# Kernel tuning notes

Measured on AMD Instinct MI355X. Metric: run time of the kernel, lower is better.

Reference implementation:

```python
import jax, jax.numpy as jnp
import numpy as np

DIM = 1024
NUM_HEADS = 16
HEAD_DIM = DIM // NUM_HEADS


def setup_inputs() -> dict:
    key = jax.random.key(0)
    ks = jax.random.split(key, 5)
    scale = 1.0 / np.sqrt(DIM)
    return {
        "x": jax.random.normal(ks[0], (2, 2048, DIM), dtype=jnp.float32),
        "qkv_w": jax.random.normal(ks[1], (3 * DIM, DIM), dtype=jnp.float32) * scale,
        "qkv_b": jax.random.normal(ks[2], (3 * DIM,), dtype=jnp.float32) * 0.01,
        "proj_w": jax.random.normal(ks[3], (DIM, DIM), dtype=jnp.float32) * scale,
        "proj_b": jax.random.normal(ks[4], (DIM,), dtype=jnp.float32) * 0.01,
    }


def reference(x, qkv_w, qkv_b, proj_w, proj_b):
    B, N, D = x.shape
    H, Hd = NUM_HEADS, HEAD_DIM
    # fused QKV projection: [B,N,3D]
    qkv = jnp.einsum('bnd,ed->bne', x, qkv_w) + qkv_b
    qkv = qkv.reshape(B, N, 3, H, Hd)
    q = qkv[:, :, 0].transpose(0, 2, 1, 3)  # [B,H,N,Hd]
    k = qkv[:, :, 1].transpose(0, 2, 1, 3)
    v = qkv[:, :, 2].transpose(0, 2, 1, 3)
    scale = 1.0 / jnp.sqrt(jnp.asarray(Hd, dtype=x.dtype))
    scores = jnp.einsum('bhqd,bhkd->bhqk', q, k) * scale  # [B,H,N,N]
    attn = jax.nn.softmax(scores, axis=-1)
    out = jnp.einsum('bhqk,bhkd->bhqd', attn, v)  # [B,H,N,Hd]
    out = out.transpose(0, 2, 1, 3).reshape(B, N, D)
    return jnp.einsum('bnd,ed->bne', out, proj_w) + proj_b
```

## Files before the change

kernel.cpp:

```cpp
#include <hip/hip_runtime.h>
#include <hip/hip_bf16.h>
#include <stdint.h>


typedef __bf16 bf16;
typedef __bf16 bf16x4 __attribute__((ext_vector_type(4)));
typedef __bf16 bf16x8 __attribute__((ext_vector_type(8)));
typedef float  f32x4  __attribute__((ext_vector_type(4)));
typedef float  f32x16 __attribute__((ext_vector_type(16)));
typedef uint32_t u32x4 __attribute__((ext_vector_type(4)));

#define QSCALE 0.18033688011112042f

__device__ __forceinline__ void gload_lds16(const void* g, void* l) {
    __builtin_amdgcn_global_load_lds(
        (const __attribute__((address_space(1))) void*)(uintptr_t)g,
        (__attribute__((address_space(3))) void*)(uint32_t)(uintptr_t)l,
        16, 0, 0);
}

__device__ __forceinline__ uint32_t pkbf(float a, float b) {
    uint16_t lo = __builtin_bit_cast(uint16_t, (bf16)a);
    uint16_t hi = __builtin_bit_cast(uint16_t, (bf16)b);
    return (uint32_t)lo | ((uint32_t)hi << 16);
}

__global__ void cast_f32_bf16(const float* __restrict__ in, bf16* __restrict__ out, int n4) {
    int i = blockIdx.x * blockDim.x + threadIdx.x;
    if (i < n4) {
        float4 v = ((const float4*)in)[i];
        bf16x4 o = { (bf16)v.x, (bf16)v.y, (bf16)v.z, (bf16)v.w };
        ((bf16x4*)out)[i] = o;
    }
}

template<int EPI>
__global__ __launch_bounds__(256) void gemm128(
    const bf16* __restrict__ A,
    const bf16* __restrict__ Bw,
    const float* __restrict__ bias,
    float* __restrict__ outF,
    bf16* __restrict__ qb, bf16* __restrict__ kf, bf16* __restrict__ vf,
    int K)
{
    __shared__ bf16 As[128 * 32];
    __shared__ bf16 Bs[128 * 32];
    __shared__ bf16 ct[EPI == 0 ? 128 * 144 : 1];
    const int tid  = threadIdx.x;
    const int lane = tid & 63, w = tid >> 6;
    const int g = lane >> 4, lr = lane & 15;
    const int wr = w >> 1, wc = w & 1;
    const int mbase = blockIdx.y * 128, nbase = blockIdx.x * 128;

    f32x4 acc[4][4] = {};

    const bf16* Ag = A  + (size_t)mbase * K;
    const bf16* Bg = Bw + (size_t)nbase * K;

    for (int kt = 0; kt < K; kt += 32) {
        {
            int c0 = tid;
            gload_lds16(Ag + (size_t)(c0 >> 2) * K + (c0 & 3) * 8, As + c0 * 8);
            gload_lds16(Bg + (size_t)(c0 >> 2) * K + (c0 & 3) * 8, Bs + c0 * 8);
            int c1 = 256 + tid;
            gload_lds16(Ag + (size_t)(c1 >> 2) * K + (c1 & 3) * 8, As + c1 * 8);
            gload_lds16(Bg + (size_t)(c1 >> 2) * K + (c1 & 3) * 8, Bs + c1 * 8);
        }
        __syncthreads();
        bf16x8 af[4], bfr[4];
        #pragma unroll
        for (int mi = 0; mi < 4; ++mi)
            af[mi] = *(const bf16x8*)(As + (wr * 64 + mi * 16 + lr) * 32 + g * 8);
        #pragma unroll
        for (int ni = 0; ni < 4; ++ni)
            bfr[ni] = *(const bf16x8*)(Bs + (wc * 64 + ni * 16 + lr) * 32 + g * 8);
        #pragma unroll
        for (int mi = 0; mi < 4; ++mi)
            #pragma unroll
            for (int ni = 0; ni < 4; ++ni)
                acc[mi][ni] = __builtin_amdgcn_mfma_f32_16x16x32_bf16(
                    af[mi], bfr[ni], acc[mi][ni], 0, 0, 0);
        __syncthreads();
        Ag += 32; Bg += 32;
    }

    if (EPI == 1) {
        #pragma unroll
        for (int ni = 0; ni < 4; ++ni) {
            int e = nbase + wc * 64 + ni * 16 + lr;
            float bv = bias[e];
            #pragma unroll
            for (int mi = 0; mi < 4; ++mi) {
                #pragma unroll
                for (int r = 0; r < 4; ++r) {
                    int token = mbase + wr * 64 + mi * 16 + g * 4 + r;
                    outF[(size_t)token * 1024 + e] = acc[mi][ni][r] + bv;
                }
            }
        }
    } else {
        const int sec = nbase >> 10;
        #pragma unroll
        for (int ni = 0; ni < 4; ++ni) {
            int ec = wc * 64 + ni * 16 + lr;
            float bv = bias[nbase + ec];
            #pragma unroll
            for (int mi = 0; mi < 4; ++mi) {
                #pragma unroll
                for (int r = 0; r < 4; ++r) {
                    int tl = wr * 64 + mi * 16 + g * 4 + r;
                    float v = acc[mi][ni][r] + bv;
                    if (sec == 0) v *= QSCALE;
                    int row = (sec == 2) ? ec : tl;
                    int col = (sec == 2) ? tl : ec;
                    ct[row * 144 + col] = (bf16)v;
                }
            }
        }
        __syncthreads();
        const int b  = mbase >> 11;
        const int h0 = (nbase & 1023) >> 6;
        const int mb = mbase & 2047;
        #pragma unroll
        for (int si = 0; si < 8; ++si) {
            int c   = si * 256 + tid;
            int hh  = c >> 10;
            int w10 = c & 1023;
            int bh  = b * 16 + h0 + hh;
            int lrow, lcol;
            size_t gaddr;
            bf16* dst;
            if (sec == 0) {
                int nl = w10 >> 3, d0 = (w10 & 7) * 8;
                lrow = nl; lcol = hh * 64 + d0;
                gaddr = ((size_t)bh * 2048 + mb + nl) * 64 + d0;
                dst = qb;
            } else if (sec == 1) {
                int o = w10 * 8;
                int frag = o >> 9, l = (o >> 3) & 63;
                int nl = (frag >> 2) * 32 + (l & 31);
                int d0 = (frag & 3) * 16 + (l >> 5) * 8;
                lrow = nl; lcol = hh * 64 + d0;
                gaddr = ((size_t)(bh * 64 + (mb >> 5))) * 2048 + o;
                dst = kf;
            } else {
                int o = w10 * 8;
                int n6 = o >> 12, r2 = o & 4095;
                int d5 = r2 >> 11, r3 = r2 & 2047;
                int nc = r3 >> 9,  l  = (r3 >> 3) & 63;
                int d  = d5 * 32 + (l & 31);
                int n0 = n6 * 64 + nc * 16 + (l >> 5) * 8;
                lrow = hh * 64 + d; lcol = n0;
                gaddr = ((size_t)(bh * 32 + (mb >> 6))) * 4096 + o;
                dst = vf;
            }
            *(bf16x8*)(dst + gaddr) = *(const bf16x8*)(&ct[lrow * 144 + lcol]);
        }
    }
}

__global__ __launch_bounds__(256, 2) void attn32(
    const bf16* __restrict__ Q,
    const bf16* __restrict__ Kf,
    const bf16* __restrict__ Vf,
    bf16* __restrict__ Ao,
    int Nseq)
{
    __shared__ bf16 Ks[2][4096];
    __shared__ bf16 Vs[2][4096];
    __shared__ bf16 ot[4][32][66];
    const int tid  = threadIdx.x;
    const int lane = tid & 63, w = tid >> 6;
    const int hi = lane >> 5, ql = lane & 31;
    const int bid = blockIdx.x;
    const int xcd = bid & 7, ii = bid >> 3;
    const int bh = xcd * 4 + (ii >> 4), qc = ii & 15;
    const int h = bh & 15, b = bh >> 4;
    const int q0 = qc * 128 + w * 32;

    const bf16* Qh  = Q  + (size_t)bh * Nseq * 64;
    const bf16* Kfh = Kf + (size_t)bh * Nseq * 64;
    const bf16* Vfh = Vf + (size_t)bh * Nseq * 64;

    bf16x8 qf[4];
    #pragma unroll
    for (int c = 0; c < 4; ++c)
        qf[c] = *(const bf16x8*)(Qh + (size_t)(q0 + ql) * 64 + c * 16 + hi * 8);

    f32x16 o0 = {}, o1 = {};
    f32x16 lv = {};

    auto stage = [&](int buf, int chunk) {
        const bf16* Kc = Kfh + (size_t)chunk * 4096;
        const bf16* Vc = Vfh + (size_t)chunk * 4096;
        gload_lds16(Kc + tid * 8,        &Ks[buf][tid * 8]);
        gload_lds16(Kc + 2048 + tid * 8, &Ks[buf][2048 + tid * 8]);
        gload_lds16(Vc + tid * 8,        &Vs[buf][tid * 8]);
        gload_lds16(Vc + 2048 + tid * 8, &Vs[buf][2048 + tid * 8]);
    };

    const int nchunks = Nseq >> 6;
    stage(0, 0);
    __syncthreads();

    for (int t = 0; t < nchunks; ++t) {
        const int cur = t & 1;
        if (t + 1 < nchunks) stage(cur ^ 1, t + 1);

        bf16x8 kin[8], vfr[8];
        #pragma unroll
        for (int i = 0; i < 8; ++i)
            kin[i] = *(const bf16x8*)(&Ks[cur][i * 512 + lane * 8]);
        #pragma unroll
        for (int i = 0; i < 8; ++i)
            vfr[i] = *(const bf16x8*)(&Vs[cur][i * 512 + lane * 8]);

        f32x16 s0 = {}, s1 = {};
        #pragma unroll
        for (int c = 0; c < 4; ++c) {
            s0 = __builtin_amdgcn_mfma_f32_32x32x16_bf16(kin[c],     qf[c], s0, 0, 0, 0);
            s1 = __builtin_amdgcn_mfma_f32_32x32x16_bf16(kin[4 + c], qf[c], s1, 0, 0, 0);
        }

        float p0[16], p1[16];
        #pragma unroll
        for (int r = 0; r < 16; ++r) { p0[r] = __builtin_amdgcn_exp2f(s0[r]); }
        #pragma unroll
        for (int r = 0; r < 16; ++r) { p1[r] = __builtin_amdgcn_exp2f(s1[r]); }
        #pragma unroll
        for (int r = 0; r < 16; ++r) { lv[r] += p0[r] + p1[r]; }

        bf16x8 pfr[4];
        #pragma unroll
        for (int f = 0; f < 4; ++f) {
            const float* pp = (f < 2) ? p0 : p1;
            const int base = (f & 1) * 8;
            union { uint32_t u[4]; bf16x8 v; } pw;
            #pragma unroll
            for (int wd = 0; wd < 2; ++wd) {
                uint32_t X = pkbf(pp[base + 2*wd], pp[base + 2*wd + 1]);
                uint32_t Y = pkbf(pp[base + 4 + 2*wd], pp[base + 4 + 2*wd + 1]);
                auto rr = __builtin_amdgcn_permlane32_swap((int)X, (int)Y, false, false);
                pw.u[wd]     = (uint32_t)rr[0];
                pw.u[2 + wd] = (uint32_t)rr[1];
            }
            pfr[f] = pw.v;
        }

        #pragma unroll
        for (int f = 0; f < 4; ++f) {
            o0 = __builtin_amdgcn_mfma_f32_32x32x16_bf16(vfr[f],     pfr[f], o0, 0, 0, 0);
            o1 = __builtin_amdgcn_mfma_f32_32x32x16_bf16(vfr[4 + f], pfr[f], o1, 0, 0, 0);
        }

        __syncthreads();
    }

    float lsum = lv[0];
    #pragma unroll
    for (int r = 1; r < 16; ++r) lsum += lv[r];
    lsum += __shfl_xor(lsum, 32);
    float linv = __builtin_amdgcn_rcpf(lsum);

    #pragma unroll
    for (int qd = 0; qd < 4; ++qd) {
        int dbase = 8 * qd + 4 * hi;
        *(uint32_t*)&ot[w][ql][dbase]          = pkbf(o0[4*qd] * linv,     o0[4*qd+1] * linv);
        *(uint32_t*)&ot[w][ql][dbase + 2]      = pkbf(o0[4*qd+2] * linv,   o0[4*qd+3] * linv);
        *(uint32_t*)&ot[w][ql][32 + dbase]     = pkbf(o1[4*qd] * linv,     o1[4*qd+1] * linv);
        *(uint32_t*)&ot[w][ql][32 + dbase + 2] = pkbf(o1[4*qd+2] * linv,   o1[4*qd+3] * linv);
    }
    __asm__ volatile("s_waitcnt lgkmcnt(0)" ::: "memory");
    const int t = lane >> 1, e = lane & 1;
    uint32_t rw[16];
    #pragma unroll
    for (int j = 0; j < 16; ++j) rw[j] = *(const uint32_t*)&ot[w][t][e * 32 + 2 * j];
    size_t gbase = (size_t)(b * Nseq + q0 + t) * 1024 + h * 64 + e * 32;
    #pragma unroll
    for (int v = 0; v < 4; ++v) {
        u32x4 sv = { rw[4*v], rw[4*v+1], rw[4*v+2], rw[4*v+3] };
        *(u32x4*)(Ao + gbase + v * 8) = sv;
    }
}

extern "C" void kernel_launch(void* const* d_in, const int* in_sizes, int n_in,
                              void* d_out, int out_size, void* d_ws, size_t ws_size,
                              hipStream_t stream) {
    const float* x      = (const float*)d_in[0];
    const float* qkv_w  = (const float*)d_in[1];
    const float* qkv_b  = (const float*)d_in[2];
    const float* proj_w = (const float*)d_in[3];
    const float* proj_b = (const float*)d_in[4];
    float* out = (float*)d_out;

    char* ws = (char*)d_ws;
    bf16* xb    = (bf16*)(ws);
    bf16* wqkv  = (bf16*)(ws + ((size_t)8  << 20));
    bf16* wproj = (bf16*)(ws + ((size_t)14 << 20));
    bf16* qb    = (bf16*)(ws + ((size_t)16 << 20));
    bf16* kf    = (bf16*)(ws + ((size_t)24 << 20));
    bf16* vf    = (bf16*)(ws + ((size_t)32 << 20));
    bf16* att   = (bf16*)(ws);

    cast_f32_bf16<<<dim3(4096), dim3(256), 0, stream>>>(x, xb, 4096 * 1024 / 4);
    cast_f32_bf16<<<dim3(3072), dim3(256), 0, stream>>>(qkv_w, wqkv, 3072 * 1024 / 4);
    cast_f32_bf16<<<dim3(1024), dim3(256), 0, stream>>>(proj_w, wproj, 1024 * 1024 / 4);

    gemm128<0><<<dim3(24, 32), dim3(256), 0, stream>>>(
        xb, wqkv, qkv_b, (float*)nullptr, qb, kf, vf, 1024);

    attn32<<<dim3(512), dim3(256), 0, stream>>>(qb, kf, vf, att, 2048);

    gemm128<1><<<dim3(8, 32), dim3(256), 0, stream>>>(
        att, wproj, proj_b, out, (bf16*)nullptr, (bf16*)nullptr, (bf16*)nullptr, 1024);
}
```

Baseline: 127.1 us.

## Split attention KV range across two wave groups and merge partials in LDS

Doubles the attention block to 512 threads. Each half of the block processes half of the key/value sequence with its own double-buffered LDS staging, and the two halves' unnormalized outputs and row sums are then combined through shared memory. This is a split-K style scheme meant to raise the number of waves in flight and shorten each wave's serial chunk loop, since the grid has only 512 blocks. The cost is 64KB of LDS per block, a reduction step with an extra barrier, and occupancy limited by LDS. The softmax has no running max, so the partial outputs can be summed directly.

```diff
diff --git a/kernel.cpp b/kernel.cpp
--- a/kernel.cpp
+++ b/kernel.cpp
@@ -159,24 +159,29 @@
     }
 }
 
-__global__ __launch_bounds__(256, 2) void attn32(
+__global__ __launch_bounds__(512, 4) void attn32(
     const bf16* __restrict__ Q,
     const bf16* __restrict__ Kf,
     const bf16* __restrict__ Vf,
     bf16* __restrict__ Ao,
     int Nseq)
 {
-    __shared__ bf16 Ks[2][4096];
-    __shared__ bf16 Vs[2][4096];
-    __shared__ bf16 ot[4][32][66];
+    __shared__ __align__(16) char smem[65536];
+    bf16*  KsB = (bf16*)smem;
+    bf16*  VsB = (bf16*)(smem + 32768);
+    float* xch = (float*)smem;
+    bf16*  otp = (bf16*)(smem + 36864);
+
     const int tid  = threadIdx.x;
-    const int lane = tid & 63, w = tid >> 6;
+    const int lane = tid & 63;
+    const int u    = tid >> 6;
+    const int half = u >> 2, qw = u & 3;
     const int hi = lane >> 5, ql = lane & 31;
     const int bid = blockIdx.x;
     const int xcd = bid & 7, ii = bid >> 3;
     const int bh = xcd * 4 + (ii >> 4), qc = ii & 15;
     const int h = bh & 15, b = bh >> 4;
-    const int q0 = qc * 128 + w * 32;
+    const int q0 = qc * 128 + qw * 32;
 
     const bf16* Qh  = Q  + (size_t)bh * Nseq * 64;
     const bf16* Kfh = Kf + (size_t)bh * Nseq * 64;
@@ -190,30 +195,37 @@
     f32x16 o0 = {}, o1 = {};
     f32x16 lv = {};
 
-    auto stage = [&](int buf, int chunk) {
-        const bf16* Kc = Kfh + (size_t)chunk * 4096;
-        const bf16* Vc = Vfh + (size_t)chunk * 4096;
-        gload_lds16(Kc + tid * 8,        &Ks[buf][tid * 8]);
-        gload_lds16(Kc + 2048 + tid * 8, &Ks[buf][2048 + tid * 8]);
-        gload_lds16(Vc + tid * 8,        &Vs[buf][tid * 8]);
-        gload_lds16(Vc + 2048 + tid * 8, &Vs[buf][2048 + tid * 8]);
+    const int nch = (Nseq >> 6) >> 1;
+    const int hk  = half * nch;
+
+    auto stage = [&](int buf, int t) {
+        const bf16* Kc = Kfh + (size_t)(hk + t) * 4096;
+        const bf16* Vc = Vfh + (size_t)(hk + t) * 4096;
+        bf16* kd = KsB + (half * 2 + buf) * 4096;
+        bf16* vd = VsB + (half * 2 + buf) * 4096;
+        int ht = tid & 255;
+        gload_lds16(Kc + ht * 8,        kd + ht * 8);
+        gload_lds16(Kc + 2048 + ht * 8, kd + 2048 + ht * 8);
+        gload_lds16(Vc + ht * 8,        vd + ht * 8);
+        gload_lds16(Vc + 2048 + ht * 8, vd + 2048 + ht * 8);
     };
 
-    const int nchunks = Nseq >> 6;
     stage(0, 0);
     __syncthreads();
 
-    for (int t = 0; t < nchunks; ++t) {
+    for (int t = 0; t < nch; ++t) {
         const int cur = t & 1;
-        if (t + 1 < nchunks) stage(cur ^ 1, t + 1);
-
+        if (t + 1 < nch) stage(cur ^ 1, t + 1);
+
+        const bf16* kl = KsB + (half * 2 + cur) * 4096;
+        const bf16* vl = VsB + (half * 2 + cur) * 4096;
         bf16x8 kin[8], vfr[8];
         #pragma unroll
         for (int i = 0; i < 8; ++i)
-            kin[i] = *(const bf16x8*)(&Ks[cur][i * 512 + lane * 8]);
+            kin[i] = *(const bf16x8*)(kl + i * 512 + lane * 8);
         #pragma unroll
         for (int i = 0; i < 8; ++i)
-            vfr[i] = *(const bf16x8*)(&Vs[cur][i * 512 + lane * 8]);
+            vfr[i] = *(const bf16x8*)(vl + i * 512 + lane * 8);
 
         f32x16 s0 = {}, s1 = {};
         #pragma unroll
@@ -260,26 +272,43 @@
     #pragma unroll
     for (int r = 1; r < 16; ++r) lsum += lv[r];
     lsum += __shfl_xor(lsum, 32);
-    float linv = __builtin_amdgcn_rcpf(lsum);
-
-    #pragma unroll
-    for (int qd = 0; qd < 4; ++qd) {
-        int dbase = 8 * qd + 4 * hi;
-        *(uint32_t*)&ot[w][ql][dbase]          = pkbf(o0[4*qd] * linv,     o0[4*qd+1] * linv);
-        *(uint32_t*)&ot[w][ql][dbase + 2]      = pkbf(o0[4*qd+2] * linv,   o0[4*qd+3] * linv);
-        *(uint32_t*)&ot[w][ql][32 + dbase]     = pkbf(o1[4*qd] * linv,     o1[4*qd+1] * linv);
-        *(uint32_t*)&ot[w][ql][32 + dbase + 2] = pkbf(o1[4*qd+2] * linv,   o1[4*qd+3] * linv);
-    }
-    __asm__ volatile("s_waitcnt lgkmcnt(0)" ::: "memory");
-    const int t = lane >> 1, e = lane & 1;
-    uint32_t rw[16];
-    #pragma unroll
-    for (int j = 0; j < 16; ++j) rw[j] = *(const uint32_t*)&ot[w][t][e * 32 + 2 * j];
-    size_t gbase = (size_t)(b * Nseq + q0 + t) * 1024 + h * 64 + e * 32;
-    #pragma unroll
-    for (int v = 0; v < 4; ++v) {
-        u32x4 sv = { rw[4*v], rw[4*v+1], rw[4*v+2], rw[4*v+3] };
-        *(u32x4*)(Ao + gbase + v * 8) = sv;
+
+    if (half == 1) {
+        float* xp = xch + ((size_t)(qw * 64 + lane)) * 36;
+        *(f32x16*)(xp)      = o0;
+        *(f32x16*)(xp + 16) = o1;
+        xp[32] = lsum;
+    }
+    __syncthreads();
+    if (half == 0) {
+        const float* xp = xch + ((size_t)(qw * 64 + lane)) * 36;
+        f32x16 oa = *(const f32x16*)(xp);
+        f32x16 ob = *(const f32x16*)(xp + 16);
+        o0 += oa; o1 += ob; lsum += xp[32];
+
+        float linv = __builtin_amdgcn_rcpf(lsum);
+
+        #pragma unroll
+        for (int qd = 0; qd < 4; ++qd) {
+            int dbase = 8 * qd + 4 * hi;
+            bf16* orow = otp + (qw * 32 + ql) * 66;
+            *(uint32_t*)(orow + dbase)          = pkbf(o0[4*qd] * linv,   o0[4*qd+1] * linv);
+            *(uint32_t*)(orow + dbase + 2)      = pkbf(o0[4*qd+2] * linv, o0[4*qd+3] * linv);
+            *(uint32_t*)(orow + 32 + dbase)     = pkbf(o1[4*qd] * linv,   o1[4*qd+1] * linv);
+            *(uint32_t*)(orow + 32 + dbase + 2) = pkbf(o1[4*qd+2] * linv, o1[4*qd+3] * linv);
+        }
+        __asm__ volatile("s_waitcnt lgkmcnt(0)" ::: "memory");
+        const int t = lane >> 1, e = lane & 1;
+        uint32_t rw[16];
+        #pragma unroll
+        for (int j = 0; j < 16; ++j)
+            rw[j] = *(const uint32_t*)(otp + (qw * 32 + t) * 66 + e * 32 + 2 * j);
+        size_t gbase = (size_t)(b * Nseq + q0 + t) * 1024 + h * 64 + e * 32;
+        #pragma unroll
+        for (int v = 0; v < 4; ++v) {
+            u32x4 sv = { rw[4*v], rw[4*v+1], rw[4*v+2], rw[4*v+3] };
+            *(u32x4*)(Ao + gbase + v * 8) = sv;
+        }
     }
 }
 
@@ -309,7 +338,7 @@
     gemm128<0><<<dim3(24, 32), dim3(256), 0, stream>>>(
         xb, wqkv, qkv_b, (float*)nullptr, qb, kf, vf, 1024);
 
-    attn32<<<dim3(512), dim3(256), 0, stream>>>(qb, kf, vf, att, 2048);
+    attn32<<<dim3(512), dim3(512), 0, stream>>>(qb, kf, vf, att, 2048);
 
     gemm128<1><<<dim3(8, 32), dim3(256), 0, stream>>>(
         att, wproj, proj_b, out, (bf16*)nullptr, (bf16*)nullptr, (bf16*)nullptr, 1024);
```

Measured after the change: 126.1 us. About the same (-0.7%).
